# Kernel optimization log

Hardware: AMD Instinct MI355X
Metric: run time of the kernel (lower is better)

## Reference

```python
import jax, jax.numpy as jnp
import numpy as np

N, E = 50000, 200000          # nodes, edges
S, V = 256, 128               # 256x0e scalars, 128x1o vectors -> node dim 640
EDGE_DIM, HID = 64, 256
NUM_ATOM, NUM_BOND = 16, 5
FAN_TP = S * S + V * V        # fully-connected TP fan-in for rescale


def setup_inputs() -> dict:
    key = jax.random.key(0)
    ks = jax.random.split(key, 12)
    h_final = jax.random.normal(ks[0], (N, S + 3 * V), dtype=jnp.float32)
    e_final = jax.random.normal(ks[1], (E, EDGE_DIM), dtype=jnp.float32)
    target_node_mask = jnp.ones((N,), dtype=bool)
    target_edge_mask = jnp.ones((E,), dtype=bool)
    edge_index = jax.random.randint(ks[2], (2, E), 0, N)

    def lin(k, o, i):
        return (jax.random.normal(k, (o, i), jnp.float32) / np.sqrt(i)).astype(jnp.float32)

    return {
        "h_final": h_final,
        "e_final": e_final,
        "target_node_mask": target_node_mask,
        "target_edge_mask": target_edge_mask,
        "edge_index": edge_index,
        "Ws_w": lin(ks[3], S, S),          # LinearRS on scalar irreps (with bias)
        "Ws_b": jnp.zeros((S,), jnp.float32),
        "Wv": lin(ks[4], V, V),            # LinearRS on 1o irreps (no bias)
        "Wcoord": (jax.random.normal(ks[5], (V,), jnp.float32) / np.sqrt(V)),  # 128x1o -> 1x1o
        "W_tp00": jax.random.normal(ks[6], (S, S), jnp.float32),  # 0e x 0e -> 0e path weights
        "W_tp11": jax.random.normal(ks[7], (V, V), jnp.float32),  # 1o x 1o -> 0e path weights
        "atom_W1": lin(ks[8], HID, S), "atom_b1": jnp.zeros((HID,), jnp.float32),
        "atom_W2": lin(ks[9], NUM_ATOM, HID), "atom_b2": jnp.zeros((NUM_ATOM,), jnp.float32),
        "bond_W1": lin(ks[10], HID, 1 + EDGE_DIM), "bond_b1": jnp.zeros((HID,), jnp.float32),
        "bond_W2": lin(ks[11], NUM_BOND, HID), "bond_b2": jnp.zeros((NUM_BOND,), jnp.float32),
    }


def reference(h_final, e_final, target_node_mask, target_edge_mask, edge_index,
              Ws_w, Ws_b, Wv, Wcoord, W_tp00, W_tp11,
              atom_W1, atom_b1, atom_W2, atom_b2,
              bond_W1, bond_b1, bond_W2, bond_b2):
    # --- node heads (masks are all-True here; boolean gather kept for faithfulness) ---
    x = h_final[target_node_mask]                 # [Nt, 640]
    xs = x[:, :S]                                 # scalar (0e) part [Nt, 256]
    xv = x[:, S:].reshape(-1, V, 3)               # vector (1o) part [Nt, 128, 3]

    scalar_feats = xs @ Ws_w.T + Ws_b             # node_scalar_proj (LinearRS)
    atom_type_logits = jax.nn.silu(scalar_feats @ atom_W1.T + atom_b1) @ atom_W2.T + atom_b2

    vec = jnp.einsum('nci,dc->ndi', xv, Wv)       # node_vector_proj, per-component channel mix
    predicted_r0 = jnp.einsum('nci,c->ni', vec, Wcoord)  # coord_head -> [Nt, 3]

    # --- bond head: edge gather + fully-connected tensor product to 0e ---
    ei = edge_index[:, target_edge_mask]
    row, col = ei[0], ei[1]
    hr, hc = h_final[row], h_final[col]           # [Et, 640] each
    sr, sc = hr[:, :S], hc[:, :S]
    vr = hr[:, S:].reshape(-1, V, 3)
    vc = hc[:, S:].reshape(-1, V, 3)
    # paths: 0e(x)0e->0e and 1o(x)1o->0e (dot product, CG norm 1/sqrt(3)), rescaled by fan-in
    tp = (jnp.einsum('ei,ej,ij->e', sr, sc, W_tp00)
          + jnp.einsum('eci,edi,cd->e', vr, vc, W_tp11) / np.sqrt(3.0)) / np.sqrt(FAN_TP)
    bond_in = jnp.concatenate([tp[:, None], e_final[target_edge_mask]], axis=-1)  # [Et, 65]
    bond_logits = jax.nn.silu(bond_in @ bond_W1.T + bond_b1) @ bond_W2.T + bond_b2

    return atom_type_logits, predicted_r0, bond_logits
```

## Files before the change

### kernel.cpp

```cpp
#include <hip/hip_runtime.h>

typedef unsigned short u16;
typedef unsigned int u32;
typedef float f32x4 __attribute__((ext_vector_type(4)));
typedef float f32x2 __attribute__((ext_vector_type(2)));
typedef short s16x8 __attribute__((ext_vector_type(8)));
typedef __bf16 bf16x8 __attribute__((ext_vector_type(8)));

#define NNODE 50000
#define NEDGE 200000
#define INV_SQRT3 0.57735026918962576f
#define INV_SQRT_FAN 0.0034938562148434216f

__device__ inline float b2f(u16 x) {
    unsigned u = ((unsigned)x) << 16;
    return __builtin_bit_cast(float, u);
}
__device__ inline u16 f2b(float f) {
    unsigned u = __builtin_bit_cast(unsigned, f);
    unsigned r = u + 0x7FFFu + ((u >> 16) & 1u);
    return (u16)(r >> 16);
}
__device__ inline float silu(float v) { return v / (1.f + __expf(-v)); }

__device__ inline float ld1(const void* p, long i, int m) {
    return m ? ((const float*)p)[i] : b2f(((const u16*)p)[i]);
}
__device__ inline void stout(void* o, long i, float v, int m) {
    if (m) ((float*)o)[i] = v; else ((u16*)o)[i] = f2b(v);
}

#if defined(__has_builtin)
# if __has_builtin(__builtin_amdgcn_cvt_pk_f32_fp8) && __has_builtin(__builtin_amdgcn_cvt_pk_fp8_f32)
#  define HAVE_FP8 1
# endif
#endif
#ifndef HAVE_FP8
# define HAVE_FP8 0
#endif

__device__ inline int f2e4m3_soft(float f) {
    unsigned u = __builtin_bit_cast(unsigned, f);
    int s = (u >> 24) & 0x80;
    float a = __builtin_fabsf(f);
    if (a >= 464.f) return s | 0x7E;
    if (a < 0.015625f) {
        int q = (int)(a * 512.f + 0.5f);
        return s | q;
    }
    int e = (int)((u >> 23) & 0xFF) - 127;
    unsigned m = u & 0x7FFFFF;
    unsigned mq = (m + 0x80000) >> 20;
    if (mq == 8) { mq = 0; e += 1; }
    if (e > 8) return s | 0x7E;
    return s | ((e + 7) << 3) | (int)mq;
}
__device__ inline float e4m3f_soft(int b) {
    int em = b & 0x7F;
    float v;
    if (em >> 3) {
        unsigned bits = ((unsigned)((em >> 3) + 120) << 23) | ((unsigned)(em & 7) << 20);
        v = __builtin_bit_cast(float, bits);
    } else {
        v = (float)em * 0.001953125f;
    }
    return (b & 0x80) ? -v : v;
}
__device__ inline int enc2(float a, float b) {
#if HAVE_FP8
    return __builtin_amdgcn_cvt_pk_fp8_f32(a, b, 0, false) & 0xFFFF;
#else
    return f2e4m3_soft(a) | (f2e4m3_soft(b) << 8);
#endif
}
__device__ inline unsigned char enc1(float a) { return (unsigned char)(enc2(a, a) & 0xFF); }

__device__ inline float dot8(unsigned p, unsigned x, float acc) {
#if HAVE_FP8
    f32x2 p0 = __builtin_amdgcn_cvt_pk_f32_fp8((int)p, false);
    f32x2 p1 = __builtin_amdgcn_cvt_pk_f32_fp8((int)p, true);
    f32x2 x0 = __builtin_amdgcn_cvt_pk_f32_fp8((int)x, false);
    f32x2 x1 = __builtin_amdgcn_cvt_pk_f32_fp8((int)x, true);
    return acc + p0.x * x0.x + p0.y * x0.y + p1.x * x1.x + p1.y * x1.y;
#else
    float r = acc;
#pragma unroll
    for (int i = 0; i < 4; ++i)
        r += e4m3f_soft((p >> (8 * i)) & 0xFF) * e4m3f_soft((x >> (8 * i)) & 0xFF);
    return r;
#endif
}

template <typename V>
__device__ auto mfma_sel(V a, V b, f32x4 c, int)
    -> decltype(__builtin_amdgcn_mfma_f32_16x16x32_bf16(a, b, c, 0, 0, 0)) {
    return __builtin_amdgcn_mfma_f32_16x16x32_bf16(a, b, c, 0, 0, 0);
}
template <typename V>
__device__ f32x4 mfma_sel(V a, V b, f32x4 c, long) {
    bf16x8 aa = __builtin_bit_cast(bf16x8, a);
    bf16x8 bb = __builtin_bit_cast(bf16x8, b);
    return __builtin_amdgcn_mfma_f32_16x16x32_bf16(aa, bb, c, 0, 0, 0);
}
__device__ inline f32x4 mfma_bf16(s16x8 a, s16x8 b, f32x4 c) {
    return mfma_sel(a, b, c, 0);
}

typedef __attribute__((address_space(1))) u32 AS1u32;
typedef __attribute__((address_space(3))) u32 AS3u32;
__device__ __forceinline__ void async16(const void* g, void* l) {
    __builtin_amdgcn_global_load_lds((AS1u32*)g, (AS3u32*)l, 16, 0, 0);
}

__global__ __launch_bounds__(256) void detect_k(const void* __restrict__ h, int* __restrict__ flag) {
    int t = threadIdx.x;
    u16 w = ((const u16*)h)[2 * t];
    int tb = (w >> 8) & 0x7F;
    bool pl = (tb >= 0x38 && tb <= 0x41);
    unsigned long long b = __ballot(pl);
    __shared__ int cnt[4];
    if ((t & 63) == 0) cnt[t >> 6] = __popcll(b);
    __syncthreads();
    if (t == 0) {
        int s = cnt[0] + cnt[1] + cnt[2] + cnt[3];
        flag[0] = (s < 128) ? 1 : 0;
    }
}

__global__ __launch_bounds__(256) void prep_misc_k(
    const void* __restrict__ W00, const void* __restrict__ W11,
    const void* __restrict__ bW1, const void* __restrict__ Wv,
    const void* __restrict__ Wcoord, const void* __restrict__ aW2,
    const void* __restrict__ bW2, const void* __restrict__ bb1,
    u16* __restrict__ W00T, u16* __restrict__ W1p, u16* __restrict__ W2p,
    float* __restrict__ w1tp, float* __restrict__ w_eff,
    u16* __restrict__ W2ah, u16* __restrict__ W11T, float* __restrict__ b1f,
    const int* __restrict__ mflag)
{
    const int m = *mflag;
    int u = blockIdx.x * 256 + threadIdx.x;
    if (u < 65536) {
        int j = u >> 8, i = u & 255;
        W00T[u] = f2b(ld1(W00, (long)i * 256 + j, m));
    } else if (u < 81920) {
        int v = u - 65536;
        int j = v & 7, ln = (v >> 3) & 63, tk = v >> 9;
        int tn = tk >> 1, kt = tk & 1;
        int hrow = tn * 16 + (ln & 15);
        int k = kt * 32 + (ln >> 4) * 8 + j;
        W1p[v] = f2b(ld1(bW1, (long)hrow * 65 + 1 + k, m));
    } else if (u < 86016) {
        int v = u - 81920;
        int j = v & 7, ln = (v >> 3) & 63, kt = v >> 9;
        int o = ln & 15;
        int k = kt * 32 + (ln >> 4) * 8 + j;
        W2p[v] = (o < 5) ? f2b(ld1(bW2, (long)o * 256 + k, m)) : (u16)0;
    } else if (u < 86272) {
        int hd = u - 86016;
        w1tp[hd] = ld1(bW1, (long)hd * 65, m);
    } else if (u < 86400) {
        int c = u - 86272;
        float acc = 0.f;
        for (int d = 0; d < 128; ++d)
            acc += ld1(Wcoord, d, m) * ld1(Wv, (long)d * 128 + c, m);
        w_eff[c] = acc;
    } else if (u < 90496) {
        int v = u - 86400;
        W2ah[v] = f2b(ld1(aW2, v, m));
    } else if (u < 106880) {
        int v = u - 90496;
        int d = v >> 7, c = v & 127;
        W11T[v] = f2b(ld1(W11, (long)c * 128 + d, m));
    } else if (u < 107136) {
        int hd = u - 106880;
        b1f[hd] = ld1(bb1, hd, m);
    }
}

__global__ __launch_bounds__(256) void prep_w1s_k(
    const void* __restrict__ aW1, const void* __restrict__ Wsw,
    const void* __restrict__ Wsb, const void* __restrict__ ab1,
    u16* __restrict__ W1sh, float* __restrict__ b1p,
    const int* __restrict__ mflag)
{
    const int m = *mflag;
    int hd = blockIdx.x, s = threadIdx.x;
    float a0 = 0.f, a1 = 0.f, a2 = 0.f, a3 = 0.f;
    for (int j = 0; j < 256; j += 4) {
        float w0 = ld1(aW1, (long)hd * 256 + j + 0, m);
        float w1 = ld1(aW1, (long)hd * 256 + j + 1, m);
        float w2 = ld1(aW1, (long)hd * 256 + j + 2, m);
        float w3 = ld1(aW1, (long)hd * 256 + j + 3, m);
        a0 += w0 * ld1(Wsw, (long)(j + 0) * 256 + s, m);
        a1 += w1 * ld1(Wsw, (long)(j + 1) * 256 + s, m);
        a2 += w2 * ld1(Wsw, (long)(j + 2) * 256 + s, m);
        a3 += w3 * ld1(Wsw, (long)(j + 3) * 256 + s, m);
    }
    W1sh[hd * 256 + s] = f2b((a0 + a1) + (a2 + a3));
    float pb = ld1(aW1, (long)hd * 256 + s, m) * ld1(Wsb, s, m);
#pragma unroll
    for (int off = 32; off > 0; off >>= 1) pb += __shfl_down(pb, off);
    __shared__ float red[4];
    if ((s & 63) == 0) red[s >> 6] = pb;
    __syncthreads();
    if (s == 0)
        b1p[hd] = ld1(ab1, hd, m) + red[0] + red[1] + red[2] + red[3];
}

__global__ __launch_bounds__(256) void zero_k(float4* __restrict__ p) {
    int t = blockIdx.x * 256 + threadIdx.x;
    if (t < 200000) p[t] = float4{0.f, 0.f, 0.f, 0.f};
}

__device__ __forceinline__ void gemm_core_128(
    const u16* __restrict__ Aptr, int lda,
    const u16* __restrict__ Bt, int ldb, int bcol0,
    long bm0, int K, u16* __restrict__ S, f32x4 acc[4][4])
{
    u16* As = S;
    u16* Bs = S + 8192;
    int tid = threadIdx.x;
    int lane = tid & 63, wave = tid >> 6;
    int sr = lane >> 2, sc = (lane & 3) * 8;

    auto stage = [&](int buf, int k0) {
#pragma unroll
        for (int i = 0; i < 2; ++i) {
            int row = wave * 32 + i * 16 + sr;
            async16(Bt + (long)(bcol0 + row) * ldb + k0 + sc,
                    Bs + buf * 4096 + wave * 1024 + i * 512);
            long grow = bm0 + row; if (grow >= NNODE) grow = NNODE - 1;
            async16(Aptr + grow * (long)lda + k0 + sc,
                    As + buf * 4096 + wave * 1024 + i * 512);
        }
    };

    int NT = K >> 5;
    stage(0, 0);
    __syncthreads();
    int wm = (wave & 1) * 64, wn = (wave >> 1) * 64;
    int lm = lane & 15, quad = lane >> 4;
    for (int t = 0; t < NT; ++t) {
        int cur = t & 1;
        if (t + 1 < NT) stage(cur ^ 1, (t + 1) * 32);
        const u16* Ac = As + cur * 4096;
        const u16* Bc = Bs + cur * 4096;
        s16x8 af[4], bfr[4];
#pragma unroll
        for (int q = 0; q < 4; ++q) {
            af[q]  = *(const s16x8*)(Ac + (wm + q * 16 + lm) * 32 + quad * 8);
            bfr[q] = *(const s16x8*)(Bc + (wn + q * 16 + lm) * 32 + quad * 8);
        }
#pragma unroll
        for (int i = 0; i < 4; ++i)
#pragma unroll
            for (int j = 0; j < 4; ++j)
                acc[i][j] = mfma_bf16(af[i], bfr[j], acc[i][j]);
        __syncthreads();
    }
}

__global__ __launch_bounds__(256) void gemmC_k(
    const void* __restrict__ h, const u16* __restrict__ Xs16,
    const u16* __restrict__ xvp,
    const u16* __restrict__ W1sh, const float* __restrict__ b1p,
    const u16* __restrict__ W2ah, float* __restrict__ outP,
    const u16* __restrict__ W00T, const u16* __restrict__ W11T,
    unsigned char* __restrict__ PQ8, float s00, float s11,
    const int* __restrict__ mflag)
{
    __shared__ __align__(16) u16 S[17408];
    int bid = blockIdx.x;
    int x = bid & 7, s = bid >> 3;
    int rb = (s / 7) * 8 + x, cb = s % 7;
    if (rb >= 391) return;
    const int m = *mflag;
    const u16* Ascal = m ? Xs16 : (const u16*)h;
    const int ldas = m ? 256 : 640;
    long bm0 = (long)rb * 128;

    f32x4 acc[4][4] = {};
    int tid = threadIdx.x, lane = tid & 63, wave = tid >> 6;
    int wm = (wave & 1) * 64, wn = (wave >> 1) * 64;
    int lm = lane & 15, quad = lane >> 4;

    if (cb < 2) {
        int bn0 = cb * 128;
        gemm_core_128(Ascal, ldas, W1sh, 256, bn0, bm0, 256, S, acc);
#pragma unroll
        for (int j = 0; j < 4; ++j) {
            int col = wn + j * 16 + lm;
            float bb = b1p[bn0 + col];
#pragma unroll
            for (int i = 0; i < 4; ++i)
#pragma unroll
                for (int rr = 0; rr < 4; ++rr)
                    S[(wm + i * 16 + quad * 4 + rr) * 136 + col] =
                        f2b(silu(acc[i][j][rr] + bb));
        }
        __syncthreads();
        const u16* wp = W2ah + lm * 256 + bn0;
#pragma unroll
        for (int rg = 0; rg < 2; ++rg) {
            int r0 = wave * 32 + rg * 16;
            f32x4 a2 = {0.f, 0.f, 0.f, 0.f};
#pragma unroll
            for (int k0 = 0; k0 < 128; k0 += 32) {
                s16x8 a = *(const s16x8*)(S + (r0 + lm) * 136 + k0 + quad * 8);
                s16x8 b = *(const s16x8*)(wp + k0 + quad * 8);
                a2 = mfma_bf16(a, b, a2);
            }
#pragma unroll
            for (int rr = 0; rr < 4; ++rr) {
                long grow = bm0 + r0 + quad * 4 + rr;
                if (grow < NNODE)
                    atomicAdd(outP + grow * 16 + lm, a2[rr]);
            }
        }
        return;
    }

    const bool qp = (cb >= 4);
    int z = cb - 4;
    if (qp)
        gemm_core_128(xvp + (long)z * 6400000, 128, W11T, 128, 0, bm0, 128, S, acc);
    else
        gemm_core_128(Ascal, ldas, W00T, 256, (cb - 2) * 128, bm0, 256, S, acc);

    float scale = qp ? s11 : s00;
    int colbase = qp ? (256 + z * 128) : (cb - 2) * 128;
    unsigned char* C8 = (unsigned char*)S;
#pragma unroll
    for (int j = 0; j < 4; ++j) {
        int col = wn + j * 16 + lm;
#pragma unroll
        for (int i = 0; i < 4; ++i)
#pragma unroll
            for (int rr = 0; rr < 4; ++rr) {
                int row = wm + i * 16 + quad * 4 + rr;
                C8[row * 128 + col] = enc1(scale * acc[i][j][rr]);
            }
    }
    __syncthreads();
#pragma unroll
    for (int v = 0; v < 4; ++v) {
        int idx = v * 256 + tid;
        int row = idx >> 3, seg = idx & 7;
        long grow = bm0 + row;
        if (grow < NNODE)
            *(uint4*)(PQ8 + grow * 640 + colbase + seg * 16) =
                *(const uint4*)(C8 + row * 128 + seg * 16);
    }
}

__global__ __launch_bounds__(256) void fin_atom_k(
    const float* __restrict__ outP, const void* __restrict__ b2v,
    void* __restrict__ out, const int* __restrict__ mflag)
{
    const int m = *mflag;
    int t4 = blockIdx.x * 256 + threadIdx.x;
    if (t4 >= 200000) return;
    float4 v = *(const float4*)(outP + (long)t4 * 4);
    int b0i = (t4 * 4) & 15;
    float r0 = v.x + ld1(b2v, b0i + 0, m);
    float r1 = v.y + ld1(b2v, b0i + 1, m);
    float r2 = v.z + ld1(b2v, b0i + 2, m);
    float r3 = v.w + ld1(b2v, b0i + 3, m);
    if (m) {
        *(float4*)((float*)out + (long)t4 * 4) = float4{r0, r1, r2, r3};
    } else {
        u16 pk[4] = {f2b(r0), f2b(r1), f2b(r2), f2b(r3)};
        *(ushort4*)((u16*)out + (long)t4 * 4) = *(const ushort4*)pk;
    }
}

__global__ __launch_bounds__(256) void packx8_k(
    const void* __restrict__ h, u16* __restrict__ xvp,
    const float* __restrict__ w_eff, unsigned char* __restrict__ X8,
    u16* __restrict__ Xs16, void* __restrict__ out,
    const int* __restrict__ mflag)
{
    const int m = *mflag;
    int lane = threadIdx.x & 63, w = threadIdx.x >> 6;
    int node = blockIdx.x * 4 + w;
    if (node >= NNODE) return;
    float s4[4];
    if (m) {
        float4 v = *(const float4*)((const float*)h + (long)node * 640 + lane * 4);
        s4[0] = v.x; s4[1] = v.y; s4[2] = v.z; s4[3] = v.w;
        u16 sx[4] = {f2b(s4[0]), f2b(s4[1]), f2b(s4[2]), f2b(s4[3])};
        *(ushort4*)(Xs16 + (long)node * 256 + lane * 4) = *(const ushort4*)sx;
    } else {
        ushort4 v = *(const ushort4*)((const u16*)h + (long)node * 640 + lane * 4);
        s4[0] = b2f(v.x); s4[1] = b2f(v.y); s4[2] = b2f(v.z); s4[3] = b2f(v.w);
    }
    unsigned sp = (unsigned)enc2(s4[0], s4[1]) | ((unsigned)enc2(s4[2], s4[3]) << 16);
    *(unsigned*)(X8 + (long)node * 640 + lane * 4) = sp;
    float a[6];
    if (m) {
        const float* p = (const float*)h + (long)node * 640 + 256 + lane * 6;
        float2 v0 = *(const float2*)p;
        float2 v1 = *(const float2*)(p + 2);
        float2 v2 = *(const float2*)(p + 4);
        a[0] = v0.x; a[1] = v0.y; a[2] = v1.x; a[3] = v1.y; a[4] = v2.x; a[5] = v2.y;
    } else {
        const u16* p = (const u16*)h + (long)node * 640 + 256 + lane * 6;
        ushort2 v0 = *(const ushort2*)p;
        ushort2 v1 = *(const ushort2*)(p + 2);
        ushort2 v2 = *(const ushort2*)(p + 4);
        a[0] = b2f(v0.x); a[1] = b2f(v0.y); a[2] = b2f(v1.x);
        a[3] = b2f(v1.y); a[4] = b2f(v2.x); a[5] = b2f(v2.y);
    }
#pragma unroll
    for (int z = 0; z < 3; ++z) {
        unsigned pk = (unsigned)f2b(a[z]) | ((unsigned)f2b(a[z + 3]) << 16);
        *(unsigned*)(xvp + (long)z * 6400000 + (long)node * 128 + lane * 2) = pk;
        *(unsigned short*)(X8 + (long)node * 640 + 256 + z * 128 + lane * 2) =
            (unsigned short)enc2(a[z], a[z + 3]);
    }
    float2 we = *(const float2*)(w_eff + lane * 2);
    float s0 = a[0] * we.x + a[3] * we.y;
    float s1 = a[1] * we.x + a[4] * we.y;
    float s2 = a[2] * we.x + a[5] * we.y;
#pragma unroll
    for (int off = 32; off > 0; off >>= 1) {
        s0 += __shfl_down(s0, off);
        s1 += __shfl_down(s1, off);
        s2 += __shfl_down(s2, off);
    }
    if (lane == 0) {
        stout(out, 800000L + (long)node * 3 + 0, s0, m);
        stout(out, 800000L + (long)node * 3 + 1, s1, m);
        stout(out, 800000L + (long)node * 3 + 2, s2, m);
    }
}

__global__ __launch_bounds__(256) void bond_fused_k(
    const void* __restrict__ A, const u16* __restrict__ W1p,
    const float* __restrict__ b1f, const u16* __restrict__ W2p,
    const void* __restrict__ b2v, const float* __restrict__ tp,
    const float* __restrict__ w1tp, void* __restrict__ out, long obase,
    const int* __restrict__ mflag)
{
    const int m = *mflag;
    __shared__ __align__(16) u16 hidS[4][16][264];
    int tid = threadIdx.x, lane = tid & 63, w = tid >> 6;
    int lm = lane & 15, quad = lane >> 4;
    int e0 = (blockIdx.x * 4 + w) * 16;
    s16x8 af0, af1;
    long base = (long)(e0 + lm) * 64 + quad * 8;
    if (m) {
        const float* ap = (const float*)A + base;
        float4 a0 = *(const float4*)ap,        a1 = *(const float4*)(ap + 4);
        float4 a2 = *(const float4*)(ap + 32), a3 = *(const float4*)(ap + 36);
        u16 t0[8] = {f2b(a0.x), f2b(a0.y), f2b(a0.z), f2b(a0.w),
                     f2b(a1.x), f2b(a1.y), f2b(a1.z), f2b(a1.w)};
        u16 t1[8] = {f2b(a2.x), f2b(a2.y), f2b(a2.z), f2b(a2.w),
                     f2b(a3.x), f2b(a3.y), f2b(a3.z), f2b(a3.w)};
        af0 = *(const s16x8*)t0; af1 = *(const s16x8*)t1;
    } else {
        af0 = *(const s16x8*)((const u16*)A + base);
        af1 = *(const s16x8*)((const u16*)A + base + 32);
    }
    float tpe = tp[e0 + lm];
    f32x4 acc1[16];
#pragma unroll
    for (int tn = 0; tn < 16; ++tn) {
        s16x8 b0 = *(const s16x8*)(W1p + ((tn * 2 + 0) * 64 + lane) * 8);
        s16x8 b1w = *(const s16x8*)(W1p + ((tn * 2 + 1) * 64 + lane) * 8);
        f32x4 a = {0.f, 0.f, 0.f, 0.f};
        a = mfma_bf16(b0, af0, a);
        a = mfma_bf16(b1w, af1, a);
        acc1[tn] = a;
    }
#pragma unroll
    for (int tn = 0; tn < 16; ++tn) {
        int hc0 = tn * 16 + quad * 4;
        float4 bb = *(const float4*)(b1f + hc0);
        float4 wt = *(const float4*)(w1tp + hc0);
        u16 pk[4];
        pk[0] = f2b(silu(acc1[tn][0] + bb.x + tpe * wt.x));
        pk[1] = f2b(silu(acc1[tn][1] + bb.y + tpe * wt.y));
        pk[2] = f2b(silu(acc1[tn][2] + bb.z + tpe * wt.z));
        pk[3] = f2b(silu(acc1[tn][3] + bb.w + tpe * wt.w));
        *(ushort4*)&hidS[w][lm][hc0] = *(const ushort4*)pk;
    }
    f32x4 acc2 = {0.f, 0.f, 0.f, 0.f};
#pragma unroll
    for (int kt = 0; kt < 8; ++kt) {
        s16x8 a = *(const s16x8*)&hidS[w][lm][kt * 32 + quad * 8];
        s16x8 b = *(const s16x8*)(W2p + (kt * 64 + lane) * 8);
        acc2 = mfma_bf16(a, b, acc2);
    }
    if (lm < 5) {
        float b2 = ld1(b2v, lm, m);
#pragma unroll
        for (int rr = 0; rr < 4; ++rr) {
            int e = e0 + quad * 4 + rr;
            stout(out, obase + (long)e * 5 + lm, acc2[rr] + b2, m);
        }
    }
}

__global__ __launch_bounds__(256) void tp_k(
    const int* __restrict__ ei, const unsigned char* __restrict__ PQ8,
    const unsigned char* __restrict__ X8, float* __restrict__ tp)
{
    int tid = threadIdx.x;
    int sub = tid & 15;
    int e = blockIdx.x * 16 + (tid >> 4);
    if (e >= NEDGE) return;
    int row = ei[e], col = ei[NEDGE + e];
    const unsigned char* pq = PQ8 + (long)row * 640;
    const unsigned char* xp = X8 + (long)col * 640;
    uint4 p0 = *(const uint4*)(pq + sub * 16);
    uint4 x0 = *(const uint4*)(xp + sub * 16);
    uint4 p1 = *(const uint4*)(pq + 256 + sub * 16);
    uint4 x1 = *(const uint4*)(xp + 256 + sub * 16);
    uint2 p2 = *(const uint2*)(pq + 512 + sub * 8);
    uint2 x2 = *(const uint2*)(xp + 512 + sub * 8);
    float acc = 0.f;
    acc = dot8(p0.x, x0.x, acc); acc = dot8(p0.y, x0.y, acc);
    acc = dot8(p0.z, x0.z, acc); acc = dot8(p0.w, x0.w, acc);
    acc = dot8(p1.x, x1.x, acc); acc = dot8(p1.y, x1.y, acc);
    acc = dot8(p1.z, x1.z, acc); acc = dot8(p1.w, x1.w, acc);
    acc = dot8(p2.x, x2.x, acc); acc = dot8(p2.y, x2.y, acc);
#pragma unroll
    for (int off = 8; off > 0; off >>= 1) acc += __shfl_down(acc, off);
    if (sub == 0) tp[e] = acc * 0.0625f;
}

extern "C" void kernel_launch(void* const* d_in, const int* in_sizes, int n_in,
                              void* d_out, int out_size, void* d_ws, size_t ws_size,
                              hipStream_t stream) {
    (void)in_sizes; (void)n_in; (void)out_size; (void)ws_size;
    const void* h      = d_in[0];
    const void* e_fin  = d_in[1];
    const int*  ei     = (const int*)d_in[4];
    const void* Ws_w   = d_in[5];
    const void* Ws_b   = d_in[6];
    const void* Wv     = d_in[7];
    const void* Wcoord = d_in[8];
    const void* W00    = d_in[9];
    const void* W11    = d_in[10];
    const void* aW1    = d_in[11];
    const void* ab1    = d_in[12];
    const void* aW2    = d_in[13];
    const void* ab2    = d_in[14];
    const void* bW1    = d_in[15];
    const void* bb1    = d_in[16];
    const void* bW2    = d_in[17];
    const void* bb2    = d_in[18];

    char* ws = (char*)d_ws;
    int*   mflag = (int*)(ws + 0);
    float* w1tp  = (float*)(ws + 512);
    float* w_eff = (float*)(ws + 2048);
    float* b1p   = (float*)(ws + 3072);
    u16*   W00T  = (u16*)(ws + 4096);
    u16*   W1p   = (u16*)(ws + 135168);
    u16*   W2p   = (u16*)(ws + 167936);
    u16*   W1sh  = (u16*)(ws + 176128);
    u16*   W2ah  = (u16*)(ws + 307200);
    u16*   W11T  = (u16*)(ws + 315392);
    float* tp    = (float*)(ws + 348160);
    float* b1f   = (float*)(ws + 1148160);
    char*  R     = ws + 1149184;
    unsigned char* PQ8  = (unsigned char*)R;
    unsigned char* X8   = (unsigned char*)(R + 33554432);
    u16*           xvp  = (u16*)(R + 67108864);
    u16*           Xs16 = (u16*)(R + 105906176);
    float*         outP = (float*)(R + 132120576);

    detect_k<<<1, 256, 0, stream>>>(h, mflag);
    prep_misc_k<<<419, 256, 0, stream>>>(W00, W11, bW1, Wv, Wcoord, aW2, bW2, bb1,
                                         W00T, W1p, W2p, w1tp, w_eff,
                                         W2ah, W11T, b1f, mflag);
    prep_w1s_k<<<256, 256, 0, stream>>>(aW1, Ws_w, Ws_b, ab1, W1sh, b1p, mflag);
    zero_k<<<782, 256, 0, stream>>>((float4*)outP);

    packx8_k<<<12500, 256, 0, stream>>>(h, xvp, w_eff, X8, Xs16, d_out, mflag);

    gemmC_k<<<2744, 256, 0, stream>>>(h, Xs16, xvp, W1sh, b1p, W2ah, outP,
                                      W00T, W11T, PQ8,
                                      16.f * INV_SQRT_FAN,
                                      16.f * INV_SQRT_FAN * INV_SQRT3, mflag);
    fin_atom_k<<<782, 256, 0, stream>>>(outP, ab2, d_out, mflag);

    tp_k<<<12500, 256, 0, stream>>>(ei, PQ8, X8, tp);

    bond_fused_k<<<3125, 256, 0, stream>>>(e_fin, W1p, b1f, W2p, bb2,
                                           tp, w1tp, d_out, 950000L, mflag);
}
```

Before: 448.1 us.

## Merge prep, pack, zero and tp/finalize kernels into fewer launches

Folds detect and w_eff computation into one kernel, and merges the weight prep, the W1s fold, node packing and output zeroing into a single block-indexed prep_all_k. It also merges the edge tensor-product kernel with atom finalization, and halves the bond_fused block size to 128 threads so more blocks are launched. bf16 packing switches to the v_cvt_pk_bf16_f32 instruction. The aim is to cut launch count and inter-kernel gaps. The merged kernels carry heterogeneous block roles, and the finalize step now shares a launch with the gather-heavy tp work.

```diff
diff --git a/kernel.cpp b/kernel.cpp
--- a/kernel.cpp
+++ b/kernel.cpp
@@ -91,6 +91,16 @@
 #endif
 }
 
+__device__ __forceinline__ u32 pk_bf16(float lo, float hi) {
+#if defined(__gfx950__) || defined(__gfx942__)
+    u32 r;
+    asm("v_cvt_pk_bf16_f32 %0, %1, %2" : "=v"(r) : "v"(lo), "v"(hi));
+    return r;
+#else
+    return (u32)f2b(lo) | ((u32)f2b(hi) << 16);
+#endif
+}
+
 template <typename V>
 __device__ auto mfma_sel(V a, V b, f32x4 c, int)
     -> decltype(__builtin_amdgcn_mfma_f32_16x16x32_bf16(a, b, c, 0, 0, 0)) {
@@ -112,104 +122,175 @@
     __builtin_amdgcn_global_load_lds((AS1u32*)g, (AS3u32*)l, 16, 0, 0);
 }
 
-__global__ __launch_bounds__(256) void detect_k(const void* __restrict__ h, int* __restrict__ flag) {
+__global__ __launch_bounds__(256) void detect_weff_k(
+    const void* __restrict__ h, const void* __restrict__ Wv,
+    const void* __restrict__ Wcoord, int* __restrict__ flag,
+    float* __restrict__ w_eff)
+{
+    __shared__ int cnt[4];
+    __shared__ int mfs;
     int t = threadIdx.x;
-    u16 w = ((const u16*)h)[2 * t];
-    int tb = (w >> 8) & 0x7F;
+    u16 wbits = ((const u16*)h)[2 * t];
+    int tb = (wbits >> 8) & 0x7F;
     bool pl = (tb >= 0x38 && tb <= 0x41);
     unsigned long long b = __ballot(pl);
-    __shared__ int cnt[4];
     if ((t & 63) == 0) cnt[t >> 6] = __popcll(b);
     __syncthreads();
     if (t == 0) {
         int s = cnt[0] + cnt[1] + cnt[2] + cnt[3];
-        flag[0] = (s < 128) ? 1 : 0;
-    }
-}
-
-__global__ __launch_bounds__(256) void prep_misc_k(
+        mfs = (s < 128) ? 1 : 0;
+        flag[0] = mfs;
+    }
+    __syncthreads();
+    const int m = mfs;
+    if (t < 128) {
+        float acc = 0.f;
+        for (int d = 0; d < 128; ++d)
+            acc += ld1(Wcoord, d, m) * ld1(Wv, (long)d * 128 + t, m);
+        w_eff[t] = acc;
+    }
+}
+
+__global__ __launch_bounds__(256) void prep_all_k(
+    const void* __restrict__ h,
+    const void* __restrict__ aW1, const void* __restrict__ Wsw,
+    const void* __restrict__ Wsb, const void* __restrict__ ab1,
     const void* __restrict__ W00, const void* __restrict__ W11,
-    const void* __restrict__ bW1, const void* __restrict__ Wv,
-    const void* __restrict__ Wcoord, const void* __restrict__ aW2,
+    const void* __restrict__ bW1, const void* __restrict__ aW2,
     const void* __restrict__ bW2, const void* __restrict__ bb1,
     u16* __restrict__ W00T, u16* __restrict__ W1p, u16* __restrict__ W2p,
-    float* __restrict__ w1tp, float* __restrict__ w_eff,
-    u16* __restrict__ W2ah, u16* __restrict__ W11T, float* __restrict__ b1f,
+    float* __restrict__ w1tp, u16* __restrict__ W2ah, u16* __restrict__ W11T,
+    float* __restrict__ b1f, u16* __restrict__ W1sh, float* __restrict__ b1p,
+    u16* __restrict__ xvp, const float* __restrict__ w_eff,
+    unsigned char* __restrict__ X8, u16* __restrict__ Xs16,
+    float4* __restrict__ outP4, void* __restrict__ out,
     const int* __restrict__ mflag)
 {
     const int m = *mflag;
-    int u = blockIdx.x * 256 + threadIdx.x;
-    if (u < 65536) {
-        int j = u >> 8, i = u & 255;
-        W00T[u] = f2b(ld1(W00, (long)i * 256 + j, m));
-    } else if (u < 81920) {
-        int v = u - 65536;
-        int j = v & 7, ln = (v >> 3) & 63, tk = v >> 9;
-        int tn = tk >> 1, kt = tk & 1;
-        int hrow = tn * 16 + (ln & 15);
-        int k = kt * 32 + (ln >> 4) * 8 + j;
-        W1p[v] = f2b(ld1(bW1, (long)hrow * 65 + 1 + k, m));
-    } else if (u < 86016) {
-        int v = u - 81920;
-        int j = v & 7, ln = (v >> 3) & 63, kt = v >> 9;
-        int o = ln & 15;
-        int k = kt * 32 + (ln >> 4) * 8 + j;
-        W2p[v] = (o < 5) ? f2b(ld1(bW2, (long)o * 256 + k, m)) : (u16)0;
-    } else if (u < 86272) {
-        int hd = u - 86016;
-        w1tp[hd] = ld1(bW1, (long)hd * 65, m);
-    } else if (u < 86400) {
-        int c = u - 86272;
-        float acc = 0.f;
-        for (int d = 0; d < 128; ++d)
-            acc += ld1(Wcoord, d, m) * ld1(Wv, (long)d * 128 + c, m);
-        w_eff[c] = acc;
-    } else if (u < 90496) {
-        int v = u - 86400;
-        W2ah[v] = f2b(ld1(aW2, v, m));
-    } else if (u < 106880) {
-        int v = u - 90496;
-        int d = v >> 7, c = v & 127;
-        W11T[v] = f2b(ld1(W11, (long)c * 128 + d, m));
-    } else if (u < 107136) {
-        int hd = u - 106880;
-        b1f[hd] = ld1(bb1, hd, m);
-    }
-}
-
-__global__ __launch_bounds__(256) void prep_w1s_k(
-    const void* __restrict__ aW1, const void* __restrict__ Wsw,
-    const void* __restrict__ Wsb, const void* __restrict__ ab1,
-    u16* __restrict__ W1sh, float* __restrict__ b1p,
-    const int* __restrict__ mflag)
-{
-    const int m = *mflag;
-    int hd = blockIdx.x, s = threadIdx.x;
-    float a0 = 0.f, a1 = 0.f, a2 = 0.f, a3 = 0.f;
-    for (int j = 0; j < 256; j += 4) {
-        float w0 = ld1(aW1, (long)hd * 256 + j + 0, m);
-        float w1 = ld1(aW1, (long)hd * 256 + j + 1, m);
-        float w2 = ld1(aW1, (long)hd * 256 + j + 2, m);
-        float w3 = ld1(aW1, (long)hd * 256 + j + 3, m);
-        a0 += w0 * ld1(Wsw, (long)(j + 0) * 256 + s, m);
-        a1 += w1 * ld1(Wsw, (long)(j + 1) * 256 + s, m);
-        a2 += w2 * ld1(Wsw, (long)(j + 2) * 256 + s, m);
-        a3 += w3 * ld1(Wsw, (long)(j + 3) * 256 + s, m);
-    }
-    W1sh[hd * 256 + s] = f2b((a0 + a1) + (a2 + a3));
-    float pb = ld1(aW1, (long)hd * 256 + s, m) * ld1(Wsb, s, m);
-#pragma unroll
-    for (int off = 32; off > 0; off >>= 1) pb += __shfl_down(pb, off);
-    __shared__ float red[4];
-    if ((s & 63) == 0) red[s >> 6] = pb;
-    __syncthreads();
-    if (s == 0)
-        b1p[hd] = ld1(ab1, hd, m) + red[0] + red[1] + red[2] + red[3];
-}
-
-__global__ __launch_bounds__(256) void zero_k(float4* __restrict__ p) {
-    int t = blockIdx.x * 256 + threadIdx.x;
-    if (t < 200000) p[t] = float4{0.f, 0.f, 0.f, 0.f};
+    int bid = blockIdx.x;
+    int tid = threadIdx.x;
+
+    if (bid < 256) {
+        int hd = bid, s = tid;
+        float a0 = 0.f, a1 = 0.f, a2 = 0.f, a3 = 0.f;
+        for (int j = 0; j < 256; j += 4) {
+            float w0 = ld1(aW1, (long)hd * 256 + j + 0, m);
+            float w1 = ld1(aW1, (long)hd * 256 + j + 1, m);
+            float w2 = ld1(aW1, (long)hd * 256 + j + 2, m);
+            float w3 = ld1(aW1, (long)hd * 256 + j + 3, m);
+            a0 += w0 * ld1(Wsw, (long)(j + 0) * 256 + s, m);
+            a1 += w1 * ld1(Wsw, (long)(j + 1) * 256 + s, m);
+            a2 += w2 * ld1(Wsw, (long)(j + 2) * 256 + s, m);
+            a3 += w3 * ld1(Wsw, (long)(j + 3) * 256 + s, m);
+        }
+        W1sh[hd * 256 + s] = f2b((a0 + a1) + (a2 + a3));
+        float pb = ld1(aW1, (long)hd * 256 + s, m) * ld1(Wsb, s, m);
+#pragma unroll
+        for (int off = 32; off > 0; off >>= 1) pb += __shfl_down(pb, off);
+        __shared__ float red[4];
+        if ((s & 63) == 0) red[s >> 6] = pb;
+        __syncthreads();
+        if (s == 0)
+            b1p[hd] = ld1(ab1, hd, m) + red[0] + red[1] + red[2] + red[3];
+        return;
+    }
+    bid -= 256;
+
+    if (bid < 12500) {
+        int lane = tid & 63, w = tid >> 6;
+        int node = bid * 4 + w;
+        if (node >= NNODE) return;
+        float s4[4];
+        if (m) {
+            float4 v = *(const float4*)((const float*)h + (long)node * 640 + lane * 4);
+            s4[0] = v.x; s4[1] = v.y; s4[2] = v.z; s4[3] = v.w;
+            u16 sx[4] = {f2b(s4[0]), f2b(s4[1]), f2b(s4[2]), f2b(s4[3])};
+            *(ushort4*)(Xs16 + (long)node * 256 + lane * 4) = *(const ushort4*)sx;
+        } else {
+            ushort4 v = *(const ushort4*)((const u16*)h + (long)node * 640 + lane * 4);
+            s4[0] = b2f(v.x); s4[1] = b2f(v.y); s4[2] = b2f(v.z); s4[3] = b2f(v.w);
+        }
+        unsigned sp = (unsigned)enc2(s4[0], s4[1]) | ((unsigned)enc2(s4[2], s4[3]) << 16);
+        *(unsigned*)(X8 + (long)node * 640 + lane * 4) = sp;
+        float a[6];
+        if (m) {
+            const float* p = (const float*)h + (long)node * 640 + 256 + lane * 6;
+            float2 v0 = *(const float2*)p;
+            float2 v1 = *(const float2*)(p + 2);
+            float2 v2 = *(const float2*)(p + 4);
+            a[0] = v0.x; a[1] = v0.y; a[2] = v1.x; a[3] = v1.y; a[4] = v2.x; a[5] = v2.y;
+        } else {
+            const u16* p = (const u16*)h + (long)node * 640 + 256 + lane * 6;
+            ushort2 v0 = *(const ushort2*)p;
+            ushort2 v1 = *(const ushort2*)(p + 2);
+            ushort2 v2 = *(const ushort2*)(p + 4);
+            a[0] = b2f(v0.x); a[1] = b2f(v0.y); a[2] = b2f(v1.x);
+            a[3] = b2f(v1.y); a[4] = b2f(v2.x); a[5] = b2f(v2.y);
+        }
+#pragma unroll
+        for (int z = 0; z < 3; ++z) {
+            unsigned pk = pk_bf16(a[z], a[z + 3]);
+            *(unsigned*)(xvp + (long)z * 6400000 + (long)node * 128 + lane * 2) = pk;
+            *(unsigned short*)(X8 + (long)node * 640 + 256 + z * 128 + lane * 2) =
+                (unsigned short)enc2(a[z], a[z + 3]);
+        }
+        float2 we = *(const float2*)(w_eff + lane * 2);
+        float s0 = a[0] * we.x + a[3] * we.y;
+        float s1 = a[1] * we.x + a[4] * we.y;
+        float s2 = a[2] * we.x + a[5] * we.y;
+#pragma unroll
+        for (int off = 32; off > 0; off >>= 1) {
+            s0 += __shfl_down(s0, off);
+            s1 += __shfl_down(s1, off);
+            s2 += __shfl_down(s2, off);
+        }
+        if (lane == 0) {
+            stout(out, 800000L + (long)node * 3 + 0, s0, m);
+            stout(out, 800000L + (long)node * 3 + 1, s1, m);
+            stout(out, 800000L + (long)node * 3 + 2, s2, m);
+        }
+        return;
+    }
+    bid -= 12500;
+
+    if (bid < 419) {
+        int u = bid * 256 + tid;
+        if (u < 65536) {
+            int j = u >> 8, i = u & 255;
+            W00T[u] = f2b(ld1(W00, (long)i * 256 + j, m));
+        } else if (u < 81920) {
+            int v = u - 65536;
+            int j = v & 7, ln = (v >> 3) & 63, tk = v >> 9;
+            int tn = tk >> 1, kt = tk & 1;
+            int hrow = tn * 16 + (ln & 15);
+            int k = kt * 32 + (ln >> 4) * 8 + j;
+            W1p[v] = f2b(ld1(bW1, (long)hrow * 65 + 1 + k, m));
+        } else if (u < 86016) {
+            int v = u - 81920;
+            int j = v & 7, ln = (v >> 3) & 63, kt = v >> 9;
+            int o = ln & 15;
+            int k = kt * 32 + (ln >> 4) * 8 + j;
+            W2p[v] = (o < 5) ? f2b(ld1(bW2, (long)o * 256 + k, m)) : (u16)0;
+        } else if (u < 86272) {
+            int hd = u - 86016;
+            w1tp[hd] = ld1(bW1, (long)hd * 65, m);
+        } else if (u < 90368) {
+            int v = u - 86272;
+            W2ah[v] = f2b(ld1(aW2, v, m));
+        } else if (u < 106752) {
+            int v = u - 90368;
+            int d = v >> 7, c = v & 127;
+            W11T[v] = f2b(ld1(W11, (long)c * 128 + d, m));
+        } else if (u < 107008) {
+            int hd = u - 106752;
+            b1f[hd] = ld1(bb1, hd, m);
+        }
+        return;
+    }
+    bid -= 419;
+
+    int t = bid * 256 + tid;
+    if (t < 200000) outP4[t] = float4{0.f, 0.f, 0.f, 0.f};
 }
 
 __device__ __forceinline__ void gemm_core_128(
@@ -353,12 +434,41 @@
     }
 }
 
-__global__ __launch_bounds__(256) void fin_atom_k(
+__global__ __launch_bounds__(256) void tpfin_k(
+    const int* __restrict__ ei, const unsigned char* __restrict__ PQ8,
+    const unsigned char* __restrict__ X8, float* __restrict__ tp,
     const float* __restrict__ outP, const void* __restrict__ b2v,
     void* __restrict__ out, const int* __restrict__ mflag)
 {
+    int bid = blockIdx.x;
+    int tid = threadIdx.x;
+    if (bid < 12500) {
+        int sub = tid & 15;
+        int e = bid * 16 + (tid >> 4);
+        if (e >= NEDGE) return;
+        int row = ei[e], col = ei[NEDGE + e];
+        const unsigned char* pq = PQ8 + (long)row * 640;
+        const unsigned char* xp = X8 + (long)col * 640;
+        uint4 p0 = *(const uint4*)(pq + sub * 16);
+        uint4 x0 = *(const uint4*)(xp + sub * 16);
+        uint4 p1 = *(const uint4*)(pq + 256 + sub * 16);
+        uint4 x1 = *(const uint4*)(xp + 256 + sub * 16);
+        uint2 p2 = *(const uint2*)(pq + 512 + sub * 8);
+        uint2 x2 = *(const uint2*)(xp + 512 + sub * 8);
+        float acc = 0.f;
+        acc = dot8(p0.x, x0.x, acc); acc = dot8(p0.y, x0.y, acc);
+        acc = dot8(p0.z, x0.z, acc); acc = dot8(p0.w, x0.w, acc);
+        acc = dot8(p1.x, x1.x, acc); acc = dot8(p1.y, x1.y, acc);
+        acc = dot8(p1.z, x1.z, acc); acc = dot8(p1.w, x1.w, acc);
+        acc = dot8(p2.x, x2.x, acc); acc = dot8(p2.y, x2.y, acc);
+#pragma unroll
+        for (int off = 8; off > 0; off >>= 1) acc += __shfl_down(acc, off);
+        if (sub == 0) tp[e] = acc * 0.0625f;
+        return;
+    }
+    bid -= 12500;
     const int m = *mflag;
-    int t4 = blockIdx.x * 256 + threadIdx.x;
+    int t4 = bid * 256 + tid;
     if (t4 >= 200000) return;
     float4 v = *(const float4*)(outP + (long)t4 * 4);
     int b0i = (t4 * 4) & 15;
@@ -374,68 +484,7 @@
     }
 }
 
-__global__ __launch_bounds__(256) void packx8_k(
-    const void* __restrict__ h, u16* __restrict__ xvp,
-    const float* __restrict__ w_eff, unsigned char* __restrict__ X8,
-    u16* __restrict__ Xs16, void* __restrict__ out,
-    const int* __restrict__ mflag)
-{
-    const int m = *mflag;
-    int lane = threadIdx.x & 63, w = threadIdx.x >> 6;
-    int node = blockIdx.x * 4 + w;
-    if (node >= NNODE) return;
-    float s4[4];
-    if (m) {
-        float4 v = *(const float4*)((const float*)h + (long)node * 640 + lane * 4);
-        s4[0] = v.x; s4[1] = v.y; s4[2] = v.z; s4[3] = v.w;
-        u16 sx[4] = {f2b(s4[0]), f2b(s4[1]), f2b(s4[2]), f2b(s4[3])};
-        *(ushort4*)(Xs16 + (long)node * 256 + lane * 4) = *(const ushort4*)sx;
-    } else {
-        ushort4 v = *(const ushort4*)((const u16*)h + (long)node * 640 + lane * 4);
-        s4[0] = b2f(v.x); s4[1] = b2f(v.y); s4[2] = b2f(v.z); s4[3] = b2f(v.w);
-    }
-    unsigned sp = (unsigned)enc2(s4[0], s4[1]) | ((unsigned)enc2(s4[2], s4[3]) << 16);
-    *(unsigned*)(X8 + (long)node * 640 + lane * 4) = sp;
-    float a[6];
-    if (m) {
-        const float* p = (const float*)h + (long)node * 640 + 256 + lane * 6;
-        float2 v0 = *(const float2*)p;
-        float2 v1 = *(const float2*)(p + 2);
-        float2 v2 = *(const float2*)(p + 4);
-        a[0] = v0.x; a[1] = v0.y; a[2] = v1.x; a[3] = v1.y; a[4] = v2.x; a[5] = v2.y;
-    } else {
-        const u16* p = (const u16*)h + (long)node * 640 + 256 + lane * 6;
-        ushort2 v0 = *(const ushort2*)p;
-        ushort2 v1 = *(const ushort2*)(p + 2);
-        ushort2 v2 = *(const ushort2*)(p + 4);
-        a[0] = b2f(v0.x); a[1] = b2f(v0.y); a[2] = b2f(v1.x);
-        a[3] = b2f(v1.y); a[4] = b2f(v2.x); a[5] = b2f(v2.y);
-    }
-#pragma unroll
-    for (int z = 0; z < 3; ++z) {
-        unsigned pk = (unsigned)f2b(a[z]) | ((unsigned)f2b(a[z + 3]) << 16);
-        *(unsigned*)(xvp + (long)z * 6400000 + (long)node * 128 + lane * 2) = pk;
-        *(unsigned short*)(X8 + (long)node * 640 + 256 + z * 128 + lane * 2) =
-            (unsigned short)enc2(a[z], a[z + 3]);
-    }
-    float2 we = *(const float2*)(w_eff + lane * 2);
-    float s0 = a[0] * we.x + a[3] * we.y;
-    float s1 = a[1] * we.x + a[4] * we.y;
-    float s2 = a[2] * we.x + a[5] * we.y;
-#pragma unroll
-    for (int off = 32; off > 0; off >>= 1) {
-        s0 += __shfl_down(s0, off);
-        s1 += __shfl_down(s1, off);
-        s2 += __shfl_down(s2, off);
-    }
-    if (lane == 0) {
-        stout(out, 800000L + (long)node * 3 + 0, s0, m);
-        stout(out, 800000L + (long)node * 3 + 1, s1, m);
-        stout(out, 800000L + (long)node * 3 + 2, s2, m);
-    }
-}
-
-__global__ __launch_bounds__(256) void bond_fused_k(
+__global__ __launch_bounds__(128) void bond_fused_k(
     const void* __restrict__ A, const u16* __restrict__ W1p,
     const float* __restrict__ b1f, const u16* __restrict__ W2p,
     const void* __restrict__ b2v, const float* __restrict__ tp,
@@ -443,10 +492,10 @@
     const int* __restrict__ mflag)
 {
     const int m = *mflag;
-    __shared__ __align__(16) u16 hidS[4][16][264];
+    __shared__ __align__(16) u16 hidS[2][16][264];
     int tid = threadIdx.x, lane = tid & 63, w = tid >> 6;
     int lm = lane & 15, quad = lane >> 4;
-    int e0 = (blockIdx.x * 4 + w) * 16;
+    int e0 = (blockIdx.x * 2 + w) * 16;
     s16x8 af0, af1;
     long base = (long)(e0 + lm) * 64 + quad * 8;
     if (m) {
@@ -478,12 +527,12 @@
         int hc0 = tn * 16 + quad * 4;
         float4 bb = *(const float4*)(b1f + hc0);
         float4 wt = *(const float4*)(w1tp + hc0);
-        u16 pk[4];
-        pk[0] = f2b(silu(acc1[tn][0] + bb.x + tpe * wt.x));
-        pk[1] = f2b(silu(acc1[tn][1] + bb.y + tpe * wt.y));
-        pk[2] = f2b(silu(acc1[tn][2] + bb.z + tpe * wt.z));
-        pk[3] = f2b(silu(acc1[tn][3] + bb.w + tpe * wt.w));
-        *(ushort4*)&hidS[w][lm][hc0] = *(const ushort4*)pk;
+        float f0 = silu(acc1[tn][0] + bb.x + tpe * wt.x);
+        float f1 = silu(acc1[tn][1] + bb.y + tpe * wt.y);
+        float f2 = silu(acc1[tn][2] + bb.z + tpe * wt.z);
+        float f3 = silu(acc1[tn][3] + bb.w + tpe * wt.w);
+        uint2 pk2 = make_uint2(pk_bf16(f0, f1), pk_bf16(f2, f3));
+        *(uint2*)((u16*)&hidS[w][lm][0] + hc0) = pk2;
     }
     f32x4 acc2 = {0.f, 0.f, 0.f, 0.f};
 #pragma unroll
@@ -500,34 +549,6 @@
             stout(out, obase + (long)e * 5 + lm, acc2[rr] + b2, m);
         }
     }
-}
-
-__global__ __launch_bounds__(256) void tp_k(
-    const int* __restrict__ ei, const unsigned char* __restrict__ PQ8,
-    const unsigned char* __restrict__ X8, float* __restrict__ tp)
-{
-    int tid = threadIdx.x;
-    int sub = tid & 15;
-    int e = blockIdx.x * 16 + (tid >> 4);
-    if (e >= NEDGE) return;
-    int row = ei[e], col = ei[NEDGE + e];
-    const unsigned char* pq = PQ8 + (long)row * 640;
-    const unsigned char* xp = X8 + (long)col * 640;
-    uint4 p0 = *(const uint4*)(pq + sub * 16);
-    uint4 x0 = *(const uint4*)(xp + sub * 16);
-    uint4 p1 = *(const uint4*)(pq + 256 + sub * 16);
-    uint4 x1 = *(const uint4*)(xp + 256 + sub * 16);
-    uint2 p2 = *(const uint2*)(pq + 512 + sub * 8);
-    uint2 x2 = *(const uint2*)(xp + 512 + sub * 8);
-    float acc = 0.f;
-    acc = dot8(p0.x, x0.x, acc); acc = dot8(p0.y, x0.y, acc);
-    acc = dot8(p0.z, x0.z, acc); acc = dot8(p0.w, x0.w, acc);
-    acc = dot8(p1.x, x1.x, acc); acc = dot8(p1.y, x1.y, acc);
-    acc = dot8(p1.z, x1.z, acc); acc = dot8(p1.w, x1.w, acc);
-    acc = dot8(p2.x, x2.x, acc); acc = dot8(p2.y, x2.y, acc);
-#pragma unroll
-    for (int off = 8; off > 0; off >>= 1) acc += __shfl_down(acc, off);
-    if (sub == 0) tp[e] = acc * 0.0625f;
 }
 
 extern "C" void kernel_launch(void* const* d_in, const int* in_sizes, int n_in,
@@ -572,23 +593,21 @@
     u16*           Xs16 = (u16*)(R + 105906176);
     float*         outP = (float*)(R + 132120576);
 
-    detect_k<<<1, 256, 0, stream>>>(h, mflag);
-    prep_misc_k<<<419, 256, 0, stream>>>(W00, W11, bW1, Wv, Wcoord, aW2, bW2, bb1,
-                                         W00T, W1p, W2p, w1tp, w_eff,
-                                         W2ah, W11T, b1f, mflag);
-    prep_w1s_k<<<256, 256, 0, stream>>>(aW1, Ws_w, Ws_b, ab1, W1sh, b1p, mflag);
-    zero_k<<<782, 256, 0, stream>>>((float4*)outP);
-
-    packx8_k<<<12500, 256, 0, stream>>>(h, xvp, w_eff, X8, Xs16, d_out, mflag);
+    detect_weff_k<<<1, 256, 0, stream>>>(h, Wv, Wcoord, mflag, w_eff);
+
+    prep_all_k<<<13957, 256, 0, stream>>>(h, aW1, Ws_w, Ws_b, ab1,
+                                          W00, W11, bW1, aW2, bW2, bb1,
+                                          W00T, W1p, W2p, w1tp, W2ah, W11T, b1f,
+                                          W1sh, b1p, xvp, w_eff, X8, Xs16,
+                                          (float4*)outP, d_out, mflag);
 
     gemmC_k<<<2744, 256, 0, stream>>>(h, Xs16, xvp, W1sh, b1p, W2ah, outP,
                                       W00T, W11T, PQ8,
                                       16.f * INV_SQRT_FAN,
                                       16.f * INV_SQRT_FAN * INV_SQRT3, mflag);
-    fin_atom_k<<<782, 256, 0, stream>>>(outP, ab2, d_out, mflag);
-
-    tp_k<<<12500, 256, 0, stream>>>(ei, PQ8, X8, tp);
-
-    bond_fused_k<<<3125, 256, 0, stream>>>(e_fin, W1p, b1f, W2p, bb2,
+
+    tpfin_k<<<13282, 256, 0, stream>>>(ei, PQ8, X8, tp, outP, ab2, d_out, mflag);
+
+    bond_fused_k<<<6250, 128, 0, stream>>>(e_fin, W1p, b1f, W2p, bb2,
                                            tp, w1tp, d_out, 950000L, mflag);
 }
```

Measured after the change: 419.3 us. -6.4%, faster.
